# Performance work log

Measured on AMD Instinct MI355X. Metric: run time of the kernel, lower is better.

Reference implementation:

```python
import math
import jax, jax.numpy as jnp
import numpy as np

B, S, D, H, F = 2, 2048, 1024, 16, 4096
HD = D // H
EPS = 1e-6
ALPHA, BETA = 0.5, 1.0  # SpectralActivation defaults


def setup_inputs() -> dict:
    key = jax.random.key(0)
    ks = jax.random.split(key, 24)
    init = lambda k, shape: (jax.random.normal(k, shape, jnp.float32) * 0.02)
    return {
        "x": jax.random.normal(ks[0], (B, S, D), jnp.float32),
        # attention params (W stored as [in, out], i.e. y = x @ W + b)
        "Wq": init(ks[1], (D, D)), "bq": jnp.zeros((D,), jnp.float32),
        "Wk": init(ks[2], (D, D)), "bk": jnp.zeros((D,), jnp.float32),
        "Wv": init(ks[3], (D, D)), "bv": jnp.zeros((D,), jnp.float32),
        "Wo": init(ks[4], (D, D)), "bo": jnp.zeros((D,), jnp.float32),
        "resonance": jnp.ones((H, 1, 1), jnp.float32),
        "phase": jnp.zeros((H, 1, 1), jnp.float32),
        # norm1
        "g1": jnp.ones((D,), jnp.float32), "b1": jnp.zeros((D,), jnp.float32),
        "s1": jnp.full((1,), 0.1, jnp.float32),
        # FFN
        "W1": init(ks[5], (D, F)), "bf1": jnp.zeros((F,), jnp.float32),
        "W2": init(ks[6], (F, D)), "bf2": jnp.zeros((D,), jnp.float32),
        # norm2
        "g2": jnp.ones((D,), jnp.float32), "b2": jnp.zeros((D,), jnp.float32),
        "s2": jnp.full((1,), 0.1, jnp.float32),
    }


def _harmonic_ln(x, gamma, beta, stab):
    mean = jnp.mean(x, axis=-1, keepdims=True)
    std = jnp.std(x, axis=-1, keepdims=True, ddof=1)  # torch std is unbiased
    std = std + stab * jnp.sin(std * math.pi)
    return gamma * ((x - mean) / (std + EPS)) + beta


def _spectral_act(x):
    c = math.sqrt(2.0 / math.pi)
    gelu_like = 0.5 * x * (1.0 + jnp.tanh(c * (x + 0.044715 * x ** 3)))
    return gelu_like + ALPHA * jnp.sin(BETA * x)


def _forward(x, Wq, bq, Wk, bk, Wv, bv, Wo, bo, resonance, phase,
             g1, b1, s1, W1, bf1, W2, bf2, g2, b2, s2):
    Bq, Sq, _ = x.shape
    q = (x @ Wq + bq).reshape(Bq, Sq, H, HD).transpose(0, 2, 1, 3)  # [B,H,S,hd]
    k = (x @ Wk + bk).reshape(Bq, Sq, H, HD).transpose(0, 2, 1, 3)
    v = (x @ Wv + bv).reshape(Bq, Sq, H, HD).transpose(0, 2, 1, 3)

    scores = jnp.einsum('bhqd,bhkd->bhqk', q, k) / math.sqrt(HD)  # [B,H,S,S]
    scores = scores + resonance[None] * jnp.sin(scores + phase[None])
    attn = jax.nn.softmax(scores, axis=-1)
    out = jnp.einsum('bhqk,bhkd->bhqd', attn, v)
    out = out.transpose(0, 2, 1, 3).reshape(Bq, Sq, D)
    attn_out = out @ Wo + bo

    x = _harmonic_ln(x + attn_out, g1, b1, s1)
    ff = _spectral_act(x @ W1 + bf1) @ W2 + bf2
    x = _harmonic_ln(x + ff, g2, b2, s2)
    return x


def reference(x, Wq, bq, Wk, bk, Wv, bv, Wo, bo, resonance, phase,
              g1, b1, s1, W1, bf1, W2, bf2, g2, b2, s2):
    return _forward(x, Wq, bq, Wk, bk, Wv, bv, Wo, bo, resonance, phase,
                    g1, b1, s1, W1, bf1, W2, bf2, g2, b2, s2)
```

## Files before the change

### kernel.cpp

```cpp
#include <hip/hip_runtime.h>
#include <cstdint>
#include <cstddef>


typedef float  f32x4  __attribute__((ext_vector_type(4)));
typedef __bf16 bf16x8 __attribute__((ext_vector_type(8)));
typedef unsigned short u16x8 __attribute__((ext_vector_type(8)));
typedef unsigned short u16x4 __attribute__((ext_vector_type(4)));
typedef unsigned int   u32x2 __attribute__((ext_vector_type(2)));
typedef unsigned int   u32x4 __attribute__((ext_vector_type(4)));

#define MFMA_BF16(a, b, c) __builtin_amdgcn_mfma_f32_16x16x32_bf16((a), (b), (c), 0, 0, 0)

static __device__ __forceinline__ unsigned short f32_to_bf16(float f) {
  return __builtin_bit_cast(unsigned short, (__bf16)f);
}
static __device__ __forceinline__ bf16x8 lds_frag(const unsigned short* base, int byte) {
  return __builtin_bit_cast(bf16x8, *(const u16x8*)((const char*)base + byte));
}
static __device__ __forceinline__ float spectral_act(float x) {
  const float c = 0.7978845608028654f;
  float g = 0.5f * x * (1.0f + tanhf(c * (x + 0.044715f * x * x * x)));
  return g + 0.5f * __sinf(x);
}
static __device__ __forceinline__ void gload_lds16(const void* g, void* lds) {
  __builtin_amdgcn_global_load_lds((const __attribute__((address_space(1))) unsigned int*)g,
                                   (__attribute__((address_space(3))) unsigned int*)lds,
                                   16, 0, 0);
}
static __device__ __forceinline__ u32x2 tr_read(unsigned addr) {
  u32x2 r;
  asm volatile("ds_read_b64_tr_b16 %0, %1" : "=v"(r) : "v"(addr));
  return r;
}

__global__ __launch_bounds__(256) void cvt_f32_bf16(const float* __restrict__ in,
                                                    unsigned short* __restrict__ out, int n) {
  int i = (blockIdx.x * 256 + threadIdx.x) * 4;
  if (i < n) {
    float4 v = *(const float4*)(in + i);
    u16x4 o;
    o[0] = f32_to_bf16(v.x); o[1] = f32_to_bf16(v.y);
    o[2] = f32_to_bf16(v.z); o[3] = f32_to_bf16(v.w);
    *(u16x4*)(out + i) = o;
  }
}

__global__ __launch_bounds__(256) void transpose_f32_bf16(const float* __restrict__ W,
                                                          unsigned short* __restrict__ Wt,
                                                          int K, int N) {
  __shared__ float tile[32][33];
  int tx = threadIdx.x & 31, ty = threadIdx.x >> 5;
  int k0 = blockIdx.y * 32, n0 = blockIdx.x * 32;
#pragma unroll
  for (int i = 0; i < 4; i++)
    tile[ty + i * 8][tx] = W[(size_t)(k0 + ty + i * 8) * N + n0 + tx];
  __syncthreads();
#pragma unroll
  for (int i = 0; i < 4; i++)
    Wt[(size_t)(n0 + ty + i * 8) * K + k0 + tx] = f32_to_bf16(tile[tx][ty + i * 8]);
}

template <int EPI>
__global__ __launch_bounds__(512, 2) void gemm_bt8(const unsigned short* __restrict__ Ag,
                                                   const unsigned short* __restrict__ Bt,
                                                   const float* __restrict__ bias,
                                                   unsigned short* __restrict__ Cb,
                                                   float* __restrict__ Cf,
                                                   int M, int N, int K) {
  __shared__ unsigned short As[2][256 * 64];
  __shared__ unsigned short Bs[2][256 * 64];
  const int t = threadIdx.x;
  const int lane = t & 63, w = t >> 6;
  const int wr = w >> 2, wc = w & 3;
  const int g = lane >> 4, cc = lane & 15;
  const int row0 = blockIdx.y * 256, col0 = blockIdx.x * 256;

  f32x4 acc[8][4];
#pragma unroll
  for (int mi = 0; mi < 8; mi++)
#pragma unroll
    for (int ni = 0; ni < 4; ni++) acc[mi][ni] = (f32x4){0.f, 0.f, 0.f, 0.f};

  const int nk = K >> 6;

  const int sro = w * 8 + (lane >> 3);
  const int sc8 = ((lane & 7) ^ ((lane >> 3) & 7)) * 8;

  auto stage = [&](int buf, int kt) {
#pragma unroll
    for (int i = 0; i < 4; ++i) {
      int r = i * 64 + sro;
      gload_lds16(Ag + (size_t)(row0 + r) * K + (kt << 6) + sc8,
                  &As[buf][(i * 64 + w * 8) * 64]);
    }
#pragma unroll
    for (int i = 0; i < 4; ++i) {
      int r = i * 64 + sro;
      gload_lds16(Bt + (size_t)(col0 + r) * K + (kt << 6) + sc8,
                  &Bs[buf][(i * 64 + w * 8) * 64]);
    }
  };

  stage(0, 0);
  if (nk > 1) {
    stage(1, 1);
    asm volatile("s_waitcnt vmcnt(8)" ::: "memory");
  } else {
    asm volatile("s_waitcnt vmcnt(0)" ::: "memory");
  }
  asm volatile("s_barrier" ::: "memory");

  int cur = 0;
  for (int kt = 0; kt < nk; ++kt) {
#pragma unroll
    for (int qm = 0; qm < 2; ++qm) {
      bf16x8 a[2][4];
#pragma unroll
      for (int ks = 0; ks < 2; ++ks)
#pragma unroll
        for (int i = 0; i < 4; ++i) {
          int r = wr * 128 + (qm * 4 + i) * 16 + cc;
          a[ks][i] = lds_frag(&As[cur][0], r * 128 + (((ks * 4 + g) ^ (cc & 7)) << 4));
        }
#pragma unroll
      for (int qn = 0; qn < 2; ++qn) {
        bf16x8 bb[2][2];
#pragma unroll
        for (int ks = 0; ks < 2; ++ks)
#pragma unroll
          for (int j = 0; j < 2; ++j) {
            int r = wc * 64 + (qn * 2 + j) * 16 + cc;
            bb[ks][j] = lds_frag(&Bs[cur][0], r * 128 + (((ks * 4 + g) ^ (cc & 7)) << 4));
          }
        __builtin_amdgcn_s_setprio(1);
#pragma unroll
        for (int ks = 0; ks < 2; ++ks)
#pragma unroll
          for (int i = 0; i < 4; ++i)
#pragma unroll
            for (int j = 0; j < 2; ++j)
              acc[qm * 4 + i][qn * 2 + j] =
                  MFMA_BF16(a[ks][i], bb[ks][j], acc[qm * 4 + i][qn * 2 + j]);
        __builtin_amdgcn_s_setprio(0);
      }
    }
    if (kt == nk - 1) break;
    asm volatile("s_waitcnt lgkmcnt(0)" ::: "memory");
    __builtin_amdgcn_sched_barrier(0);
    asm volatile("s_barrier" ::: "memory");
    if (kt + 2 < nk) {
      stage(cur, kt + 2);
      asm volatile("s_waitcnt vmcnt(8)" ::: "memory");
    } else {
      asm volatile("s_waitcnt vmcnt(0)" ::: "memory");
    }
    asm volatile("s_barrier" ::: "memory");
    cur ^= 1;
  }

#pragma unroll
  for (int mi = 0; mi < 8; ++mi) {
#pragma unroll
    for (int ni = 0; ni < 4; ++ni) {
      int col = col0 + wc * 64 + ni * 16 + cc;
      float bv = bias[col];
#pragma unroll
      for (int r4 = 0; r4 < 4; r4++) {
        int row = row0 + wr * 128 + mi * 16 + g * 4 + r4;
        float val = acc[mi][ni][r4] + bv;
        if (EPI == 2) val = spectral_act(val);
        if (EPI == 0 || EPI == 2) Cb[(size_t)row * N + col] = f32_to_bf16(val);
        else                      Cf[(size_t)row * N + col] = val;
      }
    }
  }
}

template <int BM, int BN, int EPI>
__global__ __launch_bounds__(256) void gemm_bt(const unsigned short* __restrict__ A,
                                               const unsigned short* __restrict__ Bt,
                                               const float* __restrict__ bias,
                                               unsigned short* __restrict__ Cb,
                                               float* __restrict__ Cf,
                                               int M, int N, int K) {
  constexpr int MI = BM / 32;
  constexpr int NI = BN / 32;
  __shared__ unsigned short As[2][BM * 32];
  __shared__ unsigned short Bs[2][BN * 32];
  const int t = threadIdx.x;
  const int lane = t & 63, w = t >> 6;
  const int wr = w >> 1, wc = w & 1;
  const int g = lane >> 4, cc = lane & 15;
  const int row0 = blockIdx.y * BM, col0 = blockIdx.x * BN;

  f32x4 acc[MI][NI];
#pragma unroll
  for (int mi = 0; mi < MI; mi++)
#pragma unroll
    for (int ni = 0; ni < NI; ni++) acc[mi][ni] = (f32x4){0.f, 0.f, 0.f, 0.f};

  const int nk = K >> 5;
  const int srow = lane >> 2;
  const int schunk = (lane & 3) ^ (srow & 3);

  auto stage = [&](int buf, int kt) {
#pragma unroll
    for (int i = 0; i < BM / 64; ++i) {
      int r = i * 64 + w * 16;
      gload_lds16(A + (size_t)(row0 + r + srow) * K + (kt << 5) + schunk * 8,
                  &As[buf][r * 32]);
    }
#pragma unroll
    for (int i = 0; i < BN / 64; ++i) {
      int r = i * 64 + w * 16;
      gload_lds16(Bt + (size_t)(col0 + r + srow) * K + (kt << 5) + schunk * 8,
                  &Bs[buf][r * 32]);
    }
  };

  stage(0, 0);
  __syncthreads();
  int cur = 0;
  for (int kt = 0; kt < nk; ++kt) {
    if (kt + 1 < nk) stage(cur ^ 1, kt + 1);

    bf16x8 af[MI], bg[NI];
#pragma unroll
    for (int mi = 0; mi < MI; mi++) {
      int r = wr * (BM / 2) + mi * 16 + cc;
      af[mi] = lds_frag(&As[cur][0], r * 64 + ((g ^ (cc & 3)) << 4));
    }
#pragma unroll
    for (int ni = 0; ni < NI; ni++) {
      int r = wc * (BN / 2) + ni * 16 + cc;
      bg[ni] = lds_frag(&Bs[cur][0], r * 64 + ((g ^ (cc & 3)) << 4));
    }
#pragma unroll
    for (int mi = 0; mi < MI; mi++)
#pragma unroll
      for (int ni = 0; ni < NI; ni++)
        acc[mi][ni] = MFMA_BF16(af[mi], bg[ni], acc[mi][ni]);

    __syncthreads();
    cur ^= 1;
  }

#pragma unroll
  for (int mi = 0; mi < MI; mi++) {
#pragma unroll
    for (int ni = 0; ni < NI; ni++) {
      int col = col0 + wc * (BN / 2) + ni * 16 + cc;
      float bv = bias[col];
#pragma unroll
      for (int r4 = 0; r4 < 4; r4++) {
        int row = row0 + wr * (BM / 2) + mi * 16 + g * 4 + r4;
        float val = acc[mi][ni][r4] + bv;
        if (EPI == 2) val = spectral_act(val);
        if (EPI == 0 || EPI == 2) Cb[(size_t)row * N + col] = f32_to_bf16(val);
        else                      Cf[(size_t)row * N + col] = val;
      }
    }
  }
}

__global__ __launch_bounds__(256) void attn_fused(const unsigned short* __restrict__ Qb,
                                                  const unsigned short* __restrict__ Kb,
                                                  const unsigned short* __restrict__ Vb,
                                                  int ld,
                                                  const float* __restrict__ resonance,
                                                  const float* __restrict__ phase,
                                                  unsigned short* __restrict__ O, int ldo) {
  constexpr int S = 2048;
  __shared__ unsigned short Ks[64 * 64];
  __shared__ unsigned short Vs[4][64 * 16];
  __shared__ unsigned short Ps[4][16 * 64];

  const int t = threadIdx.x, lane = t & 63, w = t >> 6;
  const int g = lane >> 4, cc = lane & 15;
  const int bh = blockIdx.y, b = bh >> 4, h = bh & 15;
  const int q0 = blockIdx.x * 64 + w * 16;
  const float res = resonance[h], ph = phase[h];

  const unsigned short* Qh = Qb + (size_t)b * S * ld + h * 64;
  const unsigned short* Kh = Kb + (size_t)b * S * ld + h * 64;
  const unsigned short* Vh = Vb + (size_t)b * S * ld + h * 64;

  bf16x8 qa0, qa1;
  {
    const unsigned short* qp = Qh + (size_t)(q0 + cc) * ld + g * 8;
    qa0 = __builtin_bit_cast(bf16x8, *(const u16x8*)qp);
    qa1 = __builtin_bit_cast(bf16x8, *(const u16x8*)(qp + 32));
  }

  bf16x8 ones8;
#pragma unroll
  for (int j = 0; j < 8; j++) ones8[j] = (__bf16)1.0f;

  const int krow = t >> 3, kc8 = (t & 7) * 8;
  const int vkey = t & 63, vb0 = (t >> 6) * 16;
  u16x8 kr0, kr1, vr0, vr1;

  auto issue_loads = [&](int kt) {
    const unsigned short* kp = Kh + (size_t)(kt * 64) * ld;
    kr0 = *(const u16x8*)(kp + (size_t)krow * ld + kc8);
    kr1 = *(const u16x8*)(kp + (size_t)(krow + 32) * ld + kc8);
    const unsigned short* vp = Vh + (size_t)(kt * 64 + vkey) * ld + vb0;
    vr0 = *(const u16x8*)vp;
    vr1 = *(const u16x8*)(vp + 8);
  };
  auto stage_lds = [&]() {
    *(u16x8*)((char*)Ks + ((krow * 128 + kc8 * 2) ^ ((krow & 7) << 4))) = kr0;
    int row2 = krow + 32;
    *(u16x8*)((char*)Ks + ((row2 * 128 + kc8 * 2) ^ ((row2 & 7) << 4))) = kr1;
    int sw = (vkey >> 3) & 1;
    char* vb = (char*)&Vs[t >> 6][0] + vkey * 32;
    *(u16x8*)(vb + sw * 16) = vr0;
    *(u16x8*)(vb + (1 - sw) * 16) = vr1;
  };

  const unsigned vs_base = (unsigned)(uintptr_t)(void*)&Vs[0][0];
  const unsigned tr_a = vs_base + (unsigned)((8 * g + (cc >> 2)) * 32 +
                                             (((cc & 2) >> 1) ^ (g & 1)) * 16 +
                                             (cc & 1) * 8);

  f32x4 oacc[4];
#pragma unroll
  for (int i = 0; i < 4; i++) oacc[i] = (f32x4){0.f, 0.f, 0.f, 0.f};
  float Mx[4] = {-1e30f, -1e30f, -1e30f, -1e30f};
  float Lx[4] = {0.f, 0.f, 0.f, 0.f};
  char* PsW = (char*)&Ps[w][0];

  issue_loads(0);
  for (int kt = 0; kt < S / 64; ++kt) {
    stage_lds();
    __syncthreads();
    if (kt + 1 < S / 64) issue_loads(kt + 1);

    f32x4 sacc[4];
#pragma unroll
    for (int nb = 0; nb < 4; nb++) sacc[nb] = (f32x4){0.f, 0.f, 0.f, 0.f};
#pragma unroll
    for (int nb = 0; nb < 4; nb++) {
      int key = nb * 16 + cc;
      int rb = key * 128, xr = (key & 7) << 4;
      bf16x8 k0 = lds_frag(Ks, (rb + g * 16) ^ xr);
      bf16x8 k1 = lds_frag(Ks, (rb + 64 + g * 16) ^ xr);
      sacc[nb] = MFMA_BF16(qa0, k0, sacc[nb]);
      sacc[nb] = MFMA_BF16(qa1, k1, sacc[nb]);
    }

    float sm[4] = {-1e30f, -1e30f, -1e30f, -1e30f};
#pragma unroll
    for (int nb = 0; nb < 4; nb++)
#pragma unroll
      for (int r4 = 0; r4 < 4; r4++) {
        float sv = sacc[nb][r4] * 0.125f;
        sv += res * __sinf(sv + ph);
        sacc[nb][r4] = sv;
        sm[r4] = fmaxf(sm[r4], sv);
      }
#pragma unroll
    for (int d = 1; d < 16; d <<= 1)
#pragma unroll
      for (int r4 = 0; r4 < 4; r4++) sm[r4] = fmaxf(sm[r4], __shfl_xor(sm[r4], d, 16));

    float alpha[4];
#pragma unroll
    for (int r4 = 0; r4 < 4; r4++) {
      float nm = fmaxf(Mx[r4], sm[r4]);
      alpha[r4] = __expf(Mx[r4] - nm);
      Mx[r4] = nm;
    }
#pragma unroll
    for (int nb = 0; nb < 4; nb++)
#pragma unroll
      for (int r4 = 0; r4 < 4; r4++) {
        float p = __expf(sacc[nb][r4] - Mx[r4]);
        int prow = g * 4 + r4, pcol = nb * 16 + cc;
        *(unsigned short*)(PsW + ((prow * 128 + pcol * 2) ^ ((prow & 7) << 4))) =
            f32_to_bf16(p);
      }

    bf16x8 pa0, pa1;
    {
      int xr = (cc & 7) << 4;
      pa0 = lds_frag((const unsigned short*)PsW, (cc * 128 + g * 16) ^ xr);
      pa1 = lds_frag((const unsigned short*)PsW, (cc * 128 + 64 + g * 16) ^ xr);
    }
    f32x4 pacc = (f32x4){0.f, 0.f, 0.f, 0.f};
    pacc = MFMA_BF16(pa0, ones8, pacc);
    pacc = MFMA_BF16(pa1, ones8, pacc);
#pragma unroll
    for (int r4 = 0; r4 < 4; r4++) Lx[r4] = Lx[r4] * alpha[r4] + pacc[r4];
#pragma unroll
    for (int nb2 = 0; nb2 < 4; nb2++)
#pragma unroll
      for (int r4 = 0; r4 < 4; r4++) oacc[nb2][r4] *= alpha[r4];

    u32x2 trv[4][4];
#pragma unroll
    for (int b2 = 0; b2 < 4; b2++) {
      unsigned a = tr_a + b2 * 2048;
      trv[b2][0] = tr_read(a);
      trv[b2][1] = tr_read(a + 128);
      trv[b2][2] = tr_read(a + 1024);
      trv[b2][3] = tr_read(a + 1152);
    }
    asm volatile("s_waitcnt lgkmcnt(0)" ::: "memory");
    __builtin_amdgcn_sched_barrier(0);
#pragma unroll
    for (int b2 = 0; b2 < 4; b2++) {
      bf16x8 v0 = __builtin_bit_cast(bf16x8,
          (u32x4){trv[b2][0][0], trv[b2][0][1], trv[b2][1][0], trv[b2][1][1]});
      bf16x8 v1 = __builtin_bit_cast(bf16x8,
          (u32x4){trv[b2][2][0], trv[b2][2][1], trv[b2][3][0], trv[b2][3][1]});
      oacc[b2] = MFMA_BF16(pa0, v0, oacc[b2]);
      oacc[b2] = MFMA_BF16(pa1, v1, oacc[b2]);
    }
    __syncthreads();
  }

#pragma unroll
  for (int nb2 = 0; nb2 < 4; nb2++)
#pragma unroll
    for (int r4 = 0; r4 < 4; r4++) {
      float ov = oacc[nb2][r4] / Lx[r4];
      O[(size_t)(b * S + q0 + g * 4 + r4) * ldo + h * 64 + nb2 * 16 + cc] = f32_to_bf16(ov);
    }
}

__global__ __launch_bounds__(256) void resid_harmonic_ln(const float* __restrict__ xin,
                                                         const float* __restrict__ radd,
                                                         const float* __restrict__ gamma,
                                                         const float* __restrict__ beta,
                                                         const float* __restrict__ stab,
                                                         float* __restrict__ yf,
                                                         unsigned short* __restrict__ yb) {
  const int row = blockIdx.x, t = threadIdx.x;
  const float* xr = xin + (size_t)row * 1024;
  const float* rr = radd + (size_t)row * 1024;
  float v[4], s = 0.f, ss = 0.f;
#pragma unroll
  for (int j = 0; j < 4; j++) {
    int idx = t + j * 256;
    v[j] = xr[idx] + rr[idx];
    s += v[j]; ss += v[j] * v[j];
  }
#pragma unroll
  for (int d = 1; d < 64; d <<= 1) { s += __shfl_xor(s, d); ss += __shfl_xor(ss, d); }
  __shared__ float sb[8];
  int lane = t & 63, wid = t >> 6;
  if (lane == 0) { sb[wid] = s; sb[4 + wid] = ss; }
  __syncthreads();
  s = sb[0] + sb[1] + sb[2] + sb[3];
  ss = sb[4] + sb[5] + sb[6] + sb[7];
  float mean = s * (1.f / 1024.f);
  float var = fmaxf((ss - 1024.f * mean * mean) * (1.f / 1023.f), 0.f);
  float sd = sqrtf(var);
  sd += stab[0] * sinf(sd * 3.14159265358979323846f);
  float inv = 1.f / (sd + 1e-6f);
#pragma unroll
  for (int j = 0; j < 4; j++) {
    int idx = t + j * 256;
    float y = gamma[idx] * ((v[j] - mean) * inv) + beta[idx];
    yf[(size_t)row * 1024 + idx] = y;
    if (yb) yb[(size_t)row * 1024 + idx] = f32_to_bf16(y);
  }
}

extern "C" void kernel_launch(void* const* d_in, const int* in_sizes, int n_in,
                              void* d_out, int out_size, void* d_ws, size_t ws_size,
                              hipStream_t stream) {
  const float* x    = (const float*)d_in[0];
  const float* Wq   = (const float*)d_in[1];
  const float* bq   = (const float*)d_in[2];
  const float* Wk   = (const float*)d_in[3];
  const float* bk   = (const float*)d_in[4];
  const float* Wv   = (const float*)d_in[5];
  const float* bv   = (const float*)d_in[6];
  const float* Wo   = (const float*)d_in[7];
  const float* bo   = (const float*)d_in[8];
  const float* reso = (const float*)d_in[9];
  const float* phas = (const float*)d_in[10];
  const float* g1   = (const float*)d_in[11];
  const float* b1   = (const float*)d_in[12];
  const float* s1   = (const float*)d_in[13];
  const float* W1   = (const float*)d_in[14];
  const float* bf1  = (const float*)d_in[15];
  const float* W2   = (const float*)d_in[16];
  const float* bf2  = (const float*)d_in[17];
  const float* g2   = (const float*)d_in[18];
  const float* b2   = (const float*)d_in[19];
  const float* s2   = (const float*)d_in[20];

  const int BS = 4096;

  char* ws = (char*)d_ws;
  const size_t OFF_QKV  = 0;
  const size_t OFF_XB   = 25165824;
  const size_t OFF_WQKV = 33554432;
  const size_t OFF_WOT  = 39845888;
  const size_t OFF_W1T  = 41943040;
  const size_t OFF_W2T  = 50331648;
  const size_t OFF_BQKV = 58720256;
  const size_t OFF_T0   = 58736640;
  const size_t OFF_X1   = 75513856;
  const size_t OFF_X1B  = 92291072;

  unsigned short* qkv   = (unsigned short*)(ws + OFF_QKV);
  unsigned short* xb    = (unsigned short*)(ws + OFF_XB);
  unsigned short* ao    = (unsigned short*)(ws + OFF_XB);
  unsigned short* Wqkvt = (unsigned short*)(ws + OFF_WQKV);
  unsigned short* Wot   = (unsigned short*)(ws + OFF_WOT);
  unsigned short* W1t   = (unsigned short*)(ws + OFF_W1T);
  unsigned short* W2t   = (unsigned short*)(ws + OFF_W2T);
  float*          bqkv  = (float*)(ws + OFF_BQKV);
  float*          t0    = (float*)(ws + OFF_T0);
  float*          x1    = (float*)(ws + OFF_X1);
  unsigned short* x1b   = (unsigned short*)(ws + OFF_X1B);
  unsigned short* hb    = (unsigned short*)(ws + OFF_QKV);
  float*          out   = (float*)d_out;

  cvt_f32_bf16<<<4096, 256, 0, stream>>>(x, xb, BS * 1024);

  transpose_f32_bf16<<<dim3(32, 32), 256, 0, stream>>>(Wq, Wqkvt, 1024, 1024);
  transpose_f32_bf16<<<dim3(32, 32), 256, 0, stream>>>(Wk, Wqkvt + (size_t)1024 * 1024, 1024, 1024);
  transpose_f32_bf16<<<dim3(32, 32), 256, 0, stream>>>(Wv, Wqkvt + (size_t)2048 * 1024, 1024, 1024);
  transpose_f32_bf16<<<dim3(32, 32), 256, 0, stream>>>(Wo, Wot, 1024, 1024);
  transpose_f32_bf16<<<dim3(128, 32), 256, 0, stream>>>(W1, W1t, 1024, 4096);
  transpose_f32_bf16<<<dim3(32, 128), 256, 0, stream>>>(W2, W2t, 4096, 1024);

  hipMemcpyAsync((void*)bqkv,          (const void*)bq, 1024 * 4, hipMemcpyDeviceToDevice, stream);
  hipMemcpyAsync((void*)(bqkv + 1024), (const void*)bk, 1024 * 4, hipMemcpyDeviceToDevice, stream);
  hipMemcpyAsync((void*)(bqkv + 2048), (const void*)bv, 1024 * 4, hipMemcpyDeviceToDevice, stream);

  gemm_bt8<0><<<dim3(12, 16), 512, 0, stream>>>(xb, Wqkvt, bqkv, qkv, nullptr,
                                                4096, 3072, 1024);

  attn_fused<<<dim3(32, 32), 256, 0, stream>>>(qkv, qkv + 1024, qkv + 2048, 3072,
                                               reso, phas, ao, 1024);

  gemm_bt<128, 64, 1><<<dim3(16, 32), 256, 0, stream>>>(ao, Wot, bo, nullptr, t0,
                                                        4096, 1024, 1024);

  resid_harmonic_ln<<<4096, 256, 0, stream>>>(x, t0, g1, b1, s1, x1, x1b);

  gemm_bt8<2><<<dim3(16, 16), 512, 0, stream>>>(x1b, W1t, bf1, hb, nullptr,
                                                4096, 4096, 1024);

  gemm_bt<128, 64, 1><<<dim3(16, 32), 256, 0, stream>>>(hb, W2t, bf2, nullptr, t0,
                                                        4096, 1024, 4096);

  resid_harmonic_ln<<<4096, 256, 0, stream>>>(x1, t0, g2, b2, s2, out, nullptr);
}
```

Measured before the change: 505.0 us.

## Interleave GEMM global-to-LDS staging with MFMA quadrants in 8-phase ping-pong schedule

Restructures the 256x256 GEMM main loop so each k-tile's MFMA work is split into four quadrant phases. Each phase issues a half-tile global-to-LDS load for the next buffer, and the loop is unrolled by two k-tiles. Finer-grained barriers and vmcnt waits spread memory traffic across the compute, rather than staging whole tiles between compute blocks. The cost is many more barriers per iteration. It also assumes nk is even and leans on a delicate wait-count protocol.

```diff
diff --git a/kernel.cpp b/kernel.cpp
--- a/kernel.cpp
+++ b/kernel.cpp
@@ -83,81 +83,105 @@
     for (int ni = 0; ni < 4; ni++) acc[mi][ni] = (f32x4){0.f, 0.f, 0.f, 0.f};
 
   const int nk = K >> 6;
-
-  const int sro = w * 8 + (lane >> 3);
+  const int sro8 = w * 8 + (lane >> 3);
   const int sc8 = ((lane & 7) ^ ((lane >> 3) & 7)) * 8;
 
-  auto stage = [&](int buf, int kt) {
-#pragma unroll
-    for (int i = 0; i < 4; ++i) {
-      int r = i * 64 + sro;
-      gload_lds16(Ag + (size_t)(row0 + r) * K + (kt << 6) + sc8,
-                  &As[buf][(i * 64 + w * 8) * 64]);
-    }
-#pragma unroll
-    for (int i = 0; i < 4; ++i) {
-      int r = i * 64 + sro;
-      gload_lds16(Bt + (size_t)(col0 + r) * K + (kt << 6) + sc8,
-                  &Bs[buf][(i * 64 + w * 8) * 64]);
-    }
-  };
-
-  stage(0, 0);
+  auto stageA = [&](int buf, int kt, int h) {
+#pragma unroll
+    for (int i = 0; i < 2; ++i) {
+      int rr = h * 128 + i * 64 + sro8;
+      gload_lds16(Ag + (size_t)(row0 + rr) * K + (kt << 6) + sc8,
+                  &As[buf][(h * 128 + i * 64 + w * 8) * 64]);
+    }
+  };
+  auto stageB = [&](int buf, int kt, int h) {
+#pragma unroll
+    for (int i = 0; i < 2; ++i) {
+      int rr = h * 128 + i * 64 + sro8;
+      gload_lds16(Bt + (size_t)(col0 + rr) * K + (kt << 6) + sc8,
+                  &Bs[buf][(h * 128 + i * 64 + w * 8) * 64]);
+    }
+  };
+  auto rdA = [&](int buf, int qm, bf16x8 a[2][4]) {
+#pragma unroll
+    for (int ks = 0; ks < 2; ++ks)
+#pragma unroll
+      for (int i = 0; i < 4; ++i) {
+        int r = wr * 128 + (qm * 4 + i) * 16 + cc;
+        a[ks][i] = lds_frag(&As[buf][0], r * 128 + (((ks * 4 + g) ^ (cc & 7)) << 4));
+      }
+  };
+  auto rdB = [&](int buf, int qn, bf16x8 bb[2][2]) {
+#pragma unroll
+    for (int ks = 0; ks < 2; ++ks)
+#pragma unroll
+      for (int j = 0; j < 2; ++j) {
+        int r = wc * 64 + (qn * 2 + j) * 16 + cc;
+        bb[ks][j] = lds_frag(&Bs[buf][0], r * 128 + (((ks * 4 + g) ^ (cc & 7)) << 4));
+      }
+  };
+  auto mma = [&](int qm, int qn, bf16x8 a[2][4], bf16x8 bb[2][2]) {
+    __builtin_amdgcn_s_setprio(1);
+#pragma unroll
+    for (int ks = 0; ks < 2; ++ks)
+#pragma unroll
+      for (int i = 0; i < 4; ++i)
+#pragma unroll
+        for (int j = 0; j < 2; ++j)
+          acc[qm * 4 + i][qn * 2 + j] =
+              MFMA_BF16(a[ks][i], bb[ks][j], acc[qm * 4 + i][qn * 2 + j]);
+    __builtin_amdgcn_s_setprio(0);
+  };
+
+#define SYNC_IN()  do { asm volatile("s_barrier" ::: "memory");               \
+                        asm volatile("s_waitcnt lgkmcnt(0)" ::: "memory");    \
+                        __builtin_amdgcn_sched_barrier(0); } while (0)
+#define SYNC_OUT() asm volatile("s_barrier" ::: "memory")
+
+  stageA(0, 0, 0); stageA(0, 0, 1); stageB(0, 0, 0); stageB(0, 0, 1);
   if (nk > 1) {
-    stage(1, 1);
-    asm volatile("s_waitcnt vmcnt(8)" ::: "memory");
+    stageA(1, 1, 0);
+    asm volatile("s_waitcnt vmcnt(2)" ::: "memory");
   } else {
     asm volatile("s_waitcnt vmcnt(0)" ::: "memory");
   }
   asm volatile("s_barrier" ::: "memory");
 
-  int cur = 0;
-  for (int kt = 0; kt < nk; ++kt) {
-#pragma unroll
-    for (int qm = 0; qm < 2; ++qm) {
-      bf16x8 a[2][4];
-#pragma unroll
-      for (int ks = 0; ks < 2; ++ks)
-#pragma unroll
-        for (int i = 0; i < 4; ++i) {
-          int r = wr * 128 + (qm * 4 + i) * 16 + cc;
-          a[ks][i] = lds_frag(&As[cur][0], r * 128 + (((ks * 4 + g) ^ (cc & 7)) << 4));
-        }
-#pragma unroll
-      for (int qn = 0; qn < 2; ++qn) {
-        bf16x8 bb[2][2];
-#pragma unroll
-        for (int ks = 0; ks < 2; ++ks)
-#pragma unroll
-          for (int j = 0; j < 2; ++j) {
-            int r = wc * 64 + (qn * 2 + j) * 16 + cc;
-            bb[ks][j] = lds_frag(&Bs[cur][0], r * 128 + (((ks * 4 + g) ^ (cc & 7)) << 4));
-          }
-        __builtin_amdgcn_s_setprio(1);
-#pragma unroll
-        for (int ks = 0; ks < 2; ++ks)
-#pragma unroll
-          for (int i = 0; i < 4; ++i)
-#pragma unroll
-            for (int j = 0; j < 2; ++j)
-              acc[qm * 4 + i][qn * 2 + j] =
-                  MFMA_BF16(a[ks][i], bb[ks][j], acc[qm * 4 + i][qn * 2 + j]);
-        __builtin_amdgcn_s_setprio(0);
-      }
-    }
-    if (kt == nk - 1) break;
-    asm volatile("s_waitcnt lgkmcnt(0)" ::: "memory");
-    __builtin_amdgcn_sched_barrier(0);
-    asm volatile("s_barrier" ::: "memory");
-    if (kt + 2 < nk) {
-      stage(cur, kt + 2);
-      asm volatile("s_waitcnt vmcnt(8)" ::: "memory");
-    } else {
-      asm volatile("s_waitcnt vmcnt(0)" ::: "memory");
-    }
-    asm volatile("s_barrier" ::: "memory");
-    cur ^= 1;
-  }
+  const int niter = nk >> 1;
+  for (int j = 0; j < niter; ++j) {
+    const int t0 = 2 * j, t1 = 2 * j + 1;
+    const bool s0 = (t0 + 2 < nk), s1 = (t1 + 2 < nk);
+    bf16x8 a[2][4], bb0[2][2], bb1[2][2];
+
+    rdA(0, 0, a); rdB(0, 0, bb0);
+    stageA(1, t1, 1);
+    SYNC_IN(); mma(0, 0, a, bb0); SYNC_OUT();
+    rdB(0, 1, bb1);
+    stageB(1, t1, 0);
+    SYNC_IN(); mma(0, 1, a, bb1); SYNC_OUT();
+    rdA(0, 1, a);
+    stageB(1, t1, 1);
+    SYNC_IN(); mma(1, 1, a, bb1); SYNC_OUT();
+    rdB(0, 0, bb0);
+    if (s0) { stageA(0, t0 + 2, 0); asm volatile("s_waitcnt vmcnt(2)" ::: "memory"); }
+    else    {                       asm volatile("s_waitcnt vmcnt(0)" ::: "memory"); }
+    SYNC_IN(); mma(1, 0, a, bb0); SYNC_OUT();
+
+    rdA(1, 0, a); rdB(1, 0, bb0);
+    if (s0) stageA(0, t0 + 2, 1);
+    SYNC_IN(); mma(0, 0, a, bb0); SYNC_OUT();
+    rdB(1, 1, bb1);
+    if (s0) stageB(0, t0 + 2, 0);
+    SYNC_IN(); mma(0, 1, a, bb1); SYNC_OUT();
+    rdA(1, 1, a);
+    if (s0) stageB(0, t0 + 2, 1);
+    SYNC_IN(); mma(1, 1, a, bb1); SYNC_OUT();
+    rdB(1, 0, bb0);
+    if (s1) { stageA(1, t1 + 2, 0); asm volatile("s_waitcnt vmcnt(2)" ::: "memory"); }
+    SYNC_IN(); mma(1, 0, a, bb0); SYNC_OUT();
+  }
+#undef SYNC_IN
+#undef SYNC_OUT
 
 #pragma unroll
   for (int mi = 0; mi < 8; ++mi) {
```

After: 486.2 us. 3.7% less time.
